# Kernel optimization log

Hardware: AMD Instinct MI355X
Metric: run time of the kernel (lower is better)

## Reference

```python
import jax, jax.numpy as jnp
import numpy as np

MARGIN = 0.5
BETA, GAMMA = 0.5, 0.2   # hard-coded in _get_triplet_selection_function
NUM_ANCHORS = 30          # hard-coded in select()
EPS_COS = 1e-8

B, C, D = 320, 80, 128


def setup_inputs() -> dict:
    key = jax.random.key(0)
    k1, k2, k3 = jax.random.split(key, 3)
    label = jax.random.randint(k1, (B, C), 0, 2).astype(jnp.int32)
    source = jax.random.normal(k2, (B, D), dtype=jnp.float32)
    target = jax.random.normal(k3, (B, D), dtype=jnp.float32)
    return {"label": label, "source": source, "target": target}


def _cos_distance(src, tgt):
    # F.cosine_similarity(src.unsqueeze(1), tgt, dim=-1): [B, B] sim matrix
    ns = jnp.linalg.norm(src, axis=-1)          # [B]
    nt = jnp.linalg.norm(tgt, axis=-1)          # [B]
    sim = (src @ tgt.T) / jnp.maximum(ns[:, None] * nt[None, :], EPS_COS)
    return jnp.clip(1.0 - sim, 0.0)


def _label_distances(labels_f):
    dot = labels_f @ labels_f.T                 # [B, B]
    sn = jnp.sqrt(jnp.diagonal(dot))            # [B]
    norms = sn[None, :] * sn[:, None]
    return 1.0 - jnp.minimum(1.0, dot / norms)


def _base_mask(b):
    ine = ~jnp.eye(b, dtype=bool)               # indices_not_equal
    # (a!=p) & (a!=n) & (p!=n)  ->  [B, B, B]
    return ine[:, :, None] & ine[:, None, :] & ine[None, :, :]


def _anchor_mask(fd, num_anchors):
    # select_diverse_anchors: pick the num_anchors anchors with the largest
    # mean feature distance to all other samples (most "diverse").
    diversity = jnp.mean(fd, axis=1)            # [B]
    _, idx = jax.lax.top_k(diversity, num_anchors)
    m = jnp.zeros((fd.shape[0],), dtype=bool).at[idx].set(True)
    return m[:, None, None]                     # broadcastable over (a, p, n)


def _triplet_mask(ld, beta, gamma):
    # select_triplets_smartly: (a, p) must be label-similar (dist <= gamma)
    # and (a, n) must be label-dissimilar (dist >= beta).
    pos = ld <= gamma                           # [B, B] over (a, p)
    neg = ld >= beta                            # [B, B] over (a, n)
    return pos[:, :, None] & neg[:, None, :]


def reference(label, source, target):
    fd = _cos_distance(source, target)                       # [B, B]
    ld = _label_distances(label.astype(jnp.float32))         # [B, B]
    mask = (_base_mask(fd.shape[0])
            & _anchor_mask(fd, NUM_ANCHORS)
            & _triplet_mask(ld, BETA, GAMMA))                # [B, B, B]
    # triplet_loss[a,p,n] = fd[a,p] - fd[a,n] + margin
    tl = fd[:, :, None] - fd[:, None, :] + MARGIN
    tl = jnp.clip(jnp.where(mask, tl, 0.0), 0.0)
    num_pos = jnp.sum(mask.astype(jnp.float32))
    return jnp.sum(tl) / (num_pos + 1e-4)
```

## Files before the change

### kernel.cpp

```cpp
#include <hip/hip_runtime.h>
#include <cstdint>

namespace {

constexpr int NB = 320;
constexpr int ND = 128;
constexpr int NC = 80;
constexpr int NANCH = 30;
constexpr int NW = 5;

constexpr size_t OFF_DIV  = 0;
constexpr size_t OFF_ASUM = 1280;
constexpr size_t OFF_ACNT = 3840;

__global__ __launch_bounds__(256) void k_main(
    const int* __restrict__ label,
    const float* __restrict__ src,
    const float* __restrict__ tgt,
    float* __restrict__ divr,
    double* __restrict__ asum,
    int* __restrict__ acnt)
{
    const int a = blockIdx.x;
    const int tid = threadIdx.x;
    const int w = tid >> 6, lane = tid & 63;

    __shared__ float sa[ND];
    __shared__ float snsa;
    __shared__ float red[256];
    __shared__ float fdrow[NB];
    __shared__ unsigned long long am[2];
    __shared__ unsigned long long pmask[NW], nmask[NW];
    __shared__ double wsum[4];

    if (tid < ND) sa[tid] = src[a * ND + tid];
    if (w == 0) {
        float s0 = src[a * ND + lane];
        float s1 = src[a * ND + lane + 64];
        float v = s0 * s0 + s1 * s1;
        for (int off = 32; off > 0; off >>= 1) v += __shfl_down(v, off);
        if (lane == 0) snsa = sqrtf(v);
    } else if (w == 1) {
        int l0 = label[a * NC + lane];
        int l1 = (lane < NC - 64) ? label[a * NC + 64 + lane] : 0;
        unsigned long long b0 = __ballot(l0 != 0);
        unsigned long long b1 = __ballot(l1 != 0);
        if (lane == 0) { am[0] = b0; am[1] = b1; }
    }
    __syncthreads();

    const float nsa = snsa;
    float acc = 0.f;
    for (int j = tid; j < NB; j += 256) {
        const float4* tp = reinterpret_cast<const float4*>(tgt + j * ND);
        float dot = 0.f, tn = 0.f;
#pragma unroll
        for (int d = 0; d < ND / 4; ++d) {
            float4 t = tp[d];
            dot += sa[4 * d + 0] * t.x + sa[4 * d + 1] * t.y +
                   sa[4 * d + 2] * t.z + sa[4 * d + 3] * t.w;
            tn += t.x * t.x + t.y * t.y + t.z * t.z + t.w * t.w;
        }
        float sim = dot / fmaxf(nsa * sqrtf(tn), 1e-8f);
        float f = fmaxf(1.0f - sim, 0.0f);
        fdrow[j] = f;
        acc += f;
    }
    red[tid] = acc;
    __syncthreads();
    for (int st = 128; st > 0; st >>= 1) {
        if (tid < st) red[tid] += red[tid + st];
        __syncthreads();
    }
    if (tid == 0) divr[a] = red[0] / (float)NB;

    const unsigned long long a0 = am[0], a1 = am[1];
    const float sna = sqrtf((float)(__popcll(a0) + __popcll(a1)));
#pragma unroll
    for (int it = 0; it < 2; ++it) {
        const int j = tid + 256 * it;
        if (j < NB) {
            const int4* lp = reinterpret_cast<const int4*>(label + j * NC);
            unsigned long long j0 = 0, j1 = 0;
#pragma unroll
            for (int q = 0; q < 16; ++q) {
                int4 v = lp[q];
                j0 |= (unsigned long long)(v.x != 0) << (4 * q + 0);
                j0 |= (unsigned long long)(v.y != 0) << (4 * q + 1);
                j0 |= (unsigned long long)(v.z != 0) << (4 * q + 2);
                j0 |= (unsigned long long)(v.w != 0) << (4 * q + 3);
            }
#pragma unroll
            for (int q = 16; q < 20; ++q) {
                int4 v = lp[q];
                const int b = 4 * (q - 16);
                j1 |= (unsigned long long)(v.x != 0) << (b + 0);
                j1 |= (unsigned long long)(v.y != 0) << (b + 1);
                j1 |= (unsigned long long)(v.z != 0) << (b + 2);
                j1 |= (unsigned long long)(v.w != 0) << (b + 3);
            }
            const float snj = sqrtf((float)(__popcll(j0) + __popcll(j1)));
            const float denom = sna * snj;
            const float dotf = (float)(__popcll(a0 & j0) + __popcll(a1 & j1));
            const float ld = 1.0f - fminf(1.0f, dotf / denom);
            const bool valid = (j != a) && (denom > 0.f);
            unsigned long long pb = __ballot(valid && (ld <= 0.2f));
            unsigned long long nb = __ballot(valid && (ld >= 0.5f));
            if (lane == 0) { pmask[j >> 6] = pb; nmask[j >> 6] = nb; }
        }
    }
    __syncthreads();

    double s = 0.0;
#pragma unroll
    for (int it = 0; it < 2; ++it) {
        const int j = tid + 256 * it;
        if (j < NB && ((nmask[j >> 6] >> (j & 63)) & 1ull)) {
            const float fn = fdrow[j];
#pragma unroll
            for (int wd = 0; wd < NW; ++wd) {
                unsigned long long m = pmask[wd];
                while (m) {
                    const int b = __builtin_ctzll(m);
                    m &= m - 1;
                    float v = fdrow[wd * 64 + b] - fn + 0.5f;
                    if (v > 0.f) s += (double)v;
                }
            }
        }
    }
    for (int off = 32; off > 0; off >>= 1) s += __shfl_down(s, off);
    if (lane == 0) wsum[w] = s;
    __syncthreads();
    if (tid == 0) {
        int P = 0, N = 0;
#pragma unroll
        for (int wd = 0; wd < NW; ++wd) {
            P += __popcll(pmask[wd]);
            N += __popcll(nmask[wd]);
        }
        asum[a] = wsum[0] + wsum[1] + wsum[2] + wsum[3];
        acnt[a] = P * N;
    }
}

__global__ __launch_bounds__(320) void k_final(
    const float* __restrict__ divr,
    const double* __restrict__ asum,
    const int* __restrict__ acnt,
    float* __restrict__ out)
{
    const int tid = threadIdx.x;
    __shared__ float dv[NB];
    __shared__ int alist[NANCH];
    __shared__ double sl[NANCH];
    __shared__ int cl[NANCH];

    dv[tid] = divr[tid];
    __syncthreads();

    const float ve = dv[tid];
    int rank = 0;
#pragma unroll 8
    for (int j = 0; j < NB; ++j) {
        float vj = dv[j];
        rank += (vj > ve) || (vj == ve && j < tid);
    }
    if (rank < NANCH) alist[rank] = tid;
    __syncthreads();

    if (tid < NANCH) {
        sl[tid] = asum[alist[tid]];
        cl[tid] = acnt[alist[tid]];
    }
    __syncthreads();
    if (tid == 0) {
        double S = 0.0;
        long long C = 0;
        for (int r = 0; r < NANCH; ++r) { S += sl[r]; C += cl[r]; }
        out[0] = (float)(S / ((double)C + 1e-4));
    }
}

}

extern "C" void kernel_launch(void* const* d_in, const int* in_sizes, int n_in,
                              void* d_out, int out_size, void* d_ws, size_t ws_size,
                              hipStream_t stream) {
    const int* label = (const int*)d_in[0];
    const float* src = (const float*)d_in[1];
    const float* tgt = (const float*)d_in[2];

    char* ws = (char*)d_ws;
    float* divr  = (float*)(ws + OFF_DIV);
    double* asum = (double*)(ws + OFF_ASUM);
    int* acnt    = (int*)(ws + OFF_ACNT);

    k_main <<<NB, 256, 0, stream>>>(label, src, tgt, divr, asum, acnt);
    k_final<<<1, 320, 0, stream>>>(divr, asum, acnt, (float*)d_out);
}
```

Before: 32.63 us.

## Prepack label bitmasks in a separate kernel and stage target rows through LDS

Adds a small pre-kernel that packs each label row into two 64-bit masks once, so each of the 320 blocks loads a 5 KB packed array instead of re-reading the full label matrix. The target matrix is now loaded with coalesced float4 reads into a padded LDS tile in five 64-row chunks, replacing strided per-thread row reads. The cost is an extra kernel launch, about 36 KB of extra LDS per block that may lower occupancy, and per-chunk barriers during which only one wave computes.

```diff
diff --git a/kernel.cpp b/kernel.cpp
--- a/kernel.cpp
+++ b/kernel.cpp
@@ -8,15 +8,43 @@
 constexpr int NC = 80;
 constexpr int NANCH = 30;
 constexpr int NW = 5;
+constexpr int LSTR = 129;
 
 constexpr size_t OFF_DIV  = 0;
 constexpr size_t OFF_ASUM = 1280;
 constexpr size_t OFF_ACNT = 3840;
+constexpr size_t OFF_PACK = 5120;
+
+__global__ __launch_bounds__(64) void k_pack(const int* __restrict__ label,
+                                             unsigned long long* __restrict__ packed) {
+    const int r = blockIdx.x * 64 + threadIdx.x;
+    const int4* lp = reinterpret_cast<const int4*>(label + r * NC);
+    unsigned long long j0 = 0, j1 = 0;
+#pragma unroll
+    for (int q = 0; q < 16; ++q) {
+        int4 v = lp[q];
+        j0 |= (unsigned long long)(v.x != 0) << (4 * q + 0);
+        j0 |= (unsigned long long)(v.y != 0) << (4 * q + 1);
+        j0 |= (unsigned long long)(v.z != 0) << (4 * q + 2);
+        j0 |= (unsigned long long)(v.w != 0) << (4 * q + 3);
+    }
+#pragma unroll
+    for (int q = 16; q < 20; ++q) {
+        int4 v = lp[q];
+        const int b = 4 * (q - 16);
+        j1 |= (unsigned long long)(v.x != 0) << (b + 0);
+        j1 |= (unsigned long long)(v.y != 0) << (b + 1);
+        j1 |= (unsigned long long)(v.z != 0) << (b + 2);
+        j1 |= (unsigned long long)(v.w != 0) << (b + 3);
+    }
+    packed[2 * r]     = j0;
+    packed[2 * r + 1] = j1;
+}
 
 __global__ __launch_bounds__(256) void k_main(
-    const int* __restrict__ label,
     const float* __restrict__ src,
     const float* __restrict__ tgt,
+    const unsigned long long* __restrict__ packed,
     float* __restrict__ divr,
     double* __restrict__ asum,
     int* __restrict__ acnt)
@@ -28,8 +56,9 @@
     __shared__ float sa[ND];
     __shared__ float snsa;
     __shared__ float red[256];
+    __shared__ unsigned long long pk[2 * NB];
+    __shared__ float tch[64 * LSTR];
     __shared__ float fdrow[NB];
-    __shared__ unsigned long long am[2];
     __shared__ unsigned long long pmask[NW], nmask[NW];
     __shared__ double wsum[4];
 
@@ -40,32 +69,44 @@
         float v = s0 * s0 + s1 * s1;
         for (int off = 32; off > 0; off >>= 1) v += __shfl_down(v, off);
         if (lane == 0) snsa = sqrtf(v);
-    } else if (w == 1) {
-        int l0 = label[a * NC + lane];
-        int l1 = (lane < NC - 64) ? label[a * NC + 64 + lane] : 0;
-        unsigned long long b0 = __ballot(l0 != 0);
-        unsigned long long b1 = __ballot(l1 != 0);
-        if (lane == 0) { am[0] = b0; am[1] = b1; }
-    }
-    __syncthreads();
-
+    }
+    for (int q = tid; q < 2 * NB; q += 256) pk[q] = packed[q];
+    __syncthreads();
+
+    const unsigned long long a0 = pk[2 * a], a1 = pk[2 * a + 1];
     const float nsa = snsa;
+
     float acc = 0.f;
-    for (int j = tid; j < NB; j += 256) {
-        const float4* tp = reinterpret_cast<const float4*>(tgt + j * ND);
-        float dot = 0.f, tn = 0.f;
-#pragma unroll
-        for (int d = 0; d < ND / 4; ++d) {
-            float4 t = tp[d];
-            dot += sa[4 * d + 0] * t.x + sa[4 * d + 1] * t.y +
-                   sa[4 * d + 2] * t.z + sa[4 * d + 3] * t.w;
-            tn += t.x * t.x + t.y * t.y + t.z * t.z + t.w * t.w;
-        }
-        float sim = dot / fmaxf(nsa * sqrtf(tn), 1e-8f);
-        float f = fmaxf(1.0f - sim, 0.0f);
-        fdrow[j] = f;
-        acc += f;
-    }
+    for (int c = 0; c < 5; ++c) {
+        for (int q = 0; q < 8; ++q) {
+            const int u = tid + 256 * q;
+            float4 v = reinterpret_cast<const float4*>(tgt)[c * 2048 + u];
+            const int r = u >> 5, d4 = (u & 31) << 2;
+            float* dst = &tch[r * LSTR + d4];
+            dst[0] = v.x; dst[1] = v.y; dst[2] = v.z; dst[3] = v.w;
+        }
+        __syncthreads();
+        const int j = (c < 4) ? (((tid >> 6) == c) ? tid : -1)
+                              : ((tid < 64) ? tid + 256 : -1);
+        if (j >= 0) {
+            const float* lrow = &tch[(j - (c << 6)) * LSTR];
+            float dot = 0.f, tn = 0.f;
+#pragma unroll
+            for (int d = 0; d < ND / 4; ++d) {
+                float x = lrow[4 * d + 0], y = lrow[4 * d + 1];
+                float z = lrow[4 * d + 2], t3 = lrow[4 * d + 3];
+                dot += sa[4 * d + 0] * x + sa[4 * d + 1] * y +
+                       sa[4 * d + 2] * z + sa[4 * d + 3] * t3;
+                tn += x * x + y * y + z * z + t3 * t3;
+            }
+            float sim = dot / fmaxf(nsa * sqrtf(tn), 1e-8f);
+            float f = fmaxf(1.0f - sim, 0.0f);
+            fdrow[j] = f;
+            acc += f;
+        }
+        __syncthreads();
+    }
+
     red[tid] = acc;
     __syncthreads();
     for (int st = 128; st > 0; st >>= 1) {
@@ -74,39 +115,20 @@
     }
     if (tid == 0) divr[a] = red[0] / (float)NB;
 
-    const unsigned long long a0 = am[0], a1 = am[1];
     const float sna = sqrtf((float)(__popcll(a0) + __popcll(a1)));
 #pragma unroll
     for (int it = 0; it < 2; ++it) {
-        const int j = tid + 256 * it;
-        if (j < NB) {
-            const int4* lp = reinterpret_cast<const int4*>(label + j * NC);
-            unsigned long long j0 = 0, j1 = 0;
-#pragma unroll
-            for (int q = 0; q < 16; ++q) {
-                int4 v = lp[q];
-                j0 |= (unsigned long long)(v.x != 0) << (4 * q + 0);
-                j0 |= (unsigned long long)(v.y != 0) << (4 * q + 1);
-                j0 |= (unsigned long long)(v.z != 0) << (4 * q + 2);
-                j0 |= (unsigned long long)(v.w != 0) << (4 * q + 3);
-            }
-#pragma unroll
-            for (int q = 16; q < 20; ++q) {
-                int4 v = lp[q];
-                const int b = 4 * (q - 16);
-                j1 |= (unsigned long long)(v.x != 0) << (b + 0);
-                j1 |= (unsigned long long)(v.y != 0) << (b + 1);
-                j1 |= (unsigned long long)(v.z != 0) << (b + 2);
-                j1 |= (unsigned long long)(v.w != 0) << (b + 3);
-            }
+        const int jj = tid + 256 * it;
+        if (jj < NB) {
+            const unsigned long long j0 = pk[2 * jj], j1 = pk[2 * jj + 1];
             const float snj = sqrtf((float)(__popcll(j0) + __popcll(j1)));
             const float denom = sna * snj;
             const float dotf = (float)(__popcll(a0 & j0) + __popcll(a1 & j1));
             const float ld = 1.0f - fminf(1.0f, dotf / denom);
-            const bool valid = (j != a) && (denom > 0.f);
+            const bool valid = (jj != a) && (denom > 0.f);
             unsigned long long pb = __ballot(valid && (ld <= 0.2f));
             unsigned long long nb = __ballot(valid && (ld >= 0.5f));
-            if (lane == 0) { pmask[j >> 6] = pb; nmask[j >> 6] = nb; }
+            if (lane == 0) { pmask[jj >> 6] = pb; nmask[jj >> 6] = nb; }
         }
     }
     __syncthreads();
@@ -114,9 +136,9 @@
     double s = 0.0;
 #pragma unroll
     for (int it = 0; it < 2; ++it) {
-        const int j = tid + 256 * it;
-        if (j < NB && ((nmask[j >> 6] >> (j & 63)) & 1ull)) {
-            const float fn = fdrow[j];
+        const int jj = tid + 256 * it;
+        if (jj < NB && ((nmask[jj >> 6] >> (jj & 63)) & 1ull)) {
+            const float fn = fdrow[jj];
 #pragma unroll
             for (int wd = 0; wd < NW; ++wd) {
                 unsigned long long m = pmask[wd];
@@ -195,7 +217,9 @@
     float* divr  = (float*)(ws + OFF_DIV);
     double* asum = (double*)(ws + OFF_ASUM);
     int* acnt    = (int*)(ws + OFF_ACNT);
-
-    k_main <<<NB, 256, 0, stream>>>(label, src, tgt, divr, asum, acnt);
+    unsigned long long* packed = (unsigned long long*)(ws + OFF_PACK);
+
+    k_pack <<<5, 64, 0, stream>>>(label, packed);
+    k_main <<<NB, 256, 0, stream>>>(src, tgt, packed, divr, asum, acnt);
     k_final<<<1, 320, 0, stream>>>(divr, asum, acnt, (float*)d_out);
 }
```

After: 37.44 us. +14.8%, slower.
